# Optimization experiments

Hardware: AMD Instinct MI355X
Metric: run time of the kernel (lower is better)

The kernel has to match this reference:

```python
import jax, jax.numpy as jnp
import numpy as np

N_INSTR = 16384   # total instructions across all blocks
T_TOK   = 16      # max tokens per instruction
N_BLOCKS = 512    # number of basic blocks (batch)
MAX_BLK = 64      # max instructions per block
H = 128           # hidden_size
N_TOKENS = 1024   # vocab
P_INSTR = 32      # instr_param_size
P_GLOB = 8        # global_param_size
D_WORD = 2 * H + P_INSTR + P_GLOB  # word-LSTM input dim (bi char hidden + params)


def setup_inputs() -> dict:
    key = jax.random.key(0)
    ks = jax.random.split(key, 16)
    rng = np.random.default_rng(0)

    # ragged block lengths summing exactly to N_INSTR, values in [8, 56]
    bl = np.full(N_BLOCKS, N_INSTR // N_BLOCKS, dtype=np.int64)  # avg 32
    half = N_BLOCKS // 2
    delta = rng.integers(-24, 25, size=half)
    bl[:half] += delta
    bl[half:] -= delta
    block_lens = jnp.asarray(bl, dtype=jnp.int32)

    token_lens = jnp.asarray(rng.integers(4, T_TOK + 1, size=N_INSTR), dtype=jnp.int32)
    tokens = jax.random.randint(ks[0], (N_INSTR, T_TOK), 0, N_TOKENS, dtype=jnp.int32)

    instr_params = jax.random.normal(ks[1], (N_INSTR, P_INSTR), dtype=jnp.float32)
    global_params = jax.random.normal(ks[2], (N_BLOCKS, P_GLOB), dtype=jnp.float32)

    s = 1.0 / np.sqrt(H)
    def u(k, shape):
        return jax.random.uniform(k, shape, jnp.float32, -s, s)

    emb = jax.random.normal(ks[3], (N_TOKENS, H), dtype=jnp.float32) * 0.02
    # char LSTM (input dim H), forward and backward directions; b = b_ih + b_hh
    char_Wih_f = u(ks[4], (4 * H, H)); char_Whh_f = u(ks[5], (4 * H, H)); char_b_f = u(ks[6], (4 * H,))
    char_Wih_b = u(ks[7], (4 * H, H)); char_Whh_b = u(ks[8], (4 * H, H)); char_b_b = u(ks[9], (4 * H,))
    # word LSTM (input dim D_WORD)
    word_Wih_f = u(ks[10], (4 * H, D_WORD)); word_Whh_f = u(ks[11], (4 * H, H)); word_b_f = u(ks[12], (4 * H,))
    word_Wih_b = u(ks[13], (4 * H, D_WORD)); word_Whh_b = u(ks[14], (4 * H, H)); word_b_b = u(ks[15], (4 * H,))
    kf = jax.random.fold_in(key, 123)
    final_W = u(kf, (1, 2 * H + P_GLOB)); final_b = jnp.zeros((1,), jnp.float32)

    return dict(tokens=tokens, token_lens=token_lens, block_lens=block_lens,
                instr_params=instr_params, global_params=global_params, emb=emb,
                char_Wih_f=char_Wih_f, char_Whh_f=char_Whh_f, char_b_f=char_b_f,
                char_Wih_b=char_Wih_b, char_Whh_b=char_Whh_b, char_b_b=char_b_b,
                word_Wih_f=word_Wih_f, word_Whh_f=word_Whh_f, word_b_f=word_b_f,
                word_Wih_b=word_Wih_b, word_Whh_b=word_Whh_b, word_b_b=word_b_b,
                final_W=final_W, final_b=final_b)


def _run_dir(x, mask, Wih, Whh, b):
    # x: (B, T, D), mask: (B, T) bool. Masked LSTM scan; returns final hidden (B, H).
    B = x.shape[0]
    Hh = Whh.shape[1]
    def step(carry, inp):
        h, c = carry
        xt, m = inp                      # (B, D), (B,)
        g = xt @ Wih.T + h @ Whh.T + b   # (B, 4H)
        i, f, gg, o = jnp.split(g, 4, axis=-1)  # torch gate order i,f,g,o
        i = jax.nn.sigmoid(i); f = jax.nn.sigmoid(f)
        gg = jnp.tanh(gg); o = jax.nn.sigmoid(o)
        cn = f * c + i * gg
        hn = o * jnp.tanh(cn)
        m = m[:, None]
        return (jnp.where(m, hn, h), jnp.where(m, cn, c)), None
    init = (jnp.zeros((B, Hh), x.dtype), jnp.zeros((B, Hh), x.dtype))
    (h, _), _ = jax.lax.scan(step, init, (jnp.swapaxes(x, 0, 1), mask.T))
    return h


def _bilstm_final(x, lens, Wih_f, Whh_f, b_f, Wih_b, Whh_b, b_b):
    # final hidden of a 1-layer bi-LSTM over ragged sequences (pack_padded semantics)
    T = x.shape[1]
    t_idx = jnp.arange(T)
    mask = t_idx[None, :] < lens[:, None]          # (B, T)
    h_f = _run_dir(x, mask, Wih_f, Whh_f, b_f)
    rev_idx = jnp.maximum(lens[:, None] - 1 - t_idx[None, :], 0)  # valid prefix reversed
    x_rev = jnp.take_along_axis(x, rev_idx[:, :, None], axis=1)
    h_b = _run_dir(x_rev, mask, Wih_b, Whh_b, b_b)
    return jnp.concatenate([h_f, h_b], axis=-1)    # (B, 2H)


def reference(tokens, token_lens, block_lens, instr_params, global_params, emb,
              char_Wih_f, char_Whh_f, char_b_f, char_Wih_b, char_Whh_b, char_b_b,
              word_Wih_f, word_Whh_f, word_b_f, word_Wih_b, word_Whh_b, word_b_b,
              final_W, final_b):
    n_instr = tokens.shape[0]
    # char level: per-instruction bi-LSTM over token embeddings
    x = emb[tokens]                                # (N, T_TOK, H)
    instr_h = _bilstm_final(x, token_lens, char_Wih_f, char_Whh_f, char_b_f,
                            char_Wih_b, char_Whh_b, char_b_b)      # (N, 2H)
    instrs = jnp.concatenate([instr_h, instr_params], axis=1)      # (N, 2H+P_INSTR)
    # ragged re-pack: assign each instruction to its block and position
    ends = jnp.cumsum(block_lens)
    starts = ends - block_lens
    ar = jnp.arange(n_instr)
    bid = jnp.searchsorted(ends, ar, side='right')                 # block id per instr
    pos = ar - starts[bid]                                         # position within block
    full = jnp.concatenate([instrs, global_params[bid]], axis=1)   # (N, D_WORD)
    padded = jnp.zeros((block_lens.shape[0], MAX_BLK, full.shape[1]), full.dtype)
    padded = padded.at[bid, pos].set(full)                         # (B, MAX_BLK, D_WORD)
    # word level: per-block bi-LSTM over instruction summaries
    blocks_h = _bilstm_final(padded, block_lens, word_Wih_f, word_Whh_f, word_b_f,
                             word_Wih_b, word_Whh_b, word_b_b)     # (B, 2H)
    final_in = jnp.concatenate([blocks_h, global_params], axis=1)  # (B, 2H+P_GLOB)
    return final_in @ final_W.T + final_b                          # (B, 1)
```

## Files before the change

### kernel.cpp

```cpp
#include <hip/hip_runtime.h>
#include <hip/hip_bf16.h>
#include <math.h>

#define N_INSTR   16384
#define T_TOK     16
#define N_BLOCKS  512
#define MAX_BLK   64
#define HDIM      128
#define P_INSTR   32
#define P_GLOB    8
#define D_WORD    296
#define N_TOKENS  1024

#define CIB       32

#define HPAR      131072

__device__ __forceinline__ float sigf(float x) {
    return 1.0f / (1.0f + __expf(-x));
}
__device__ __forceinline__ float tanhf_s(float x) {
    float a = fabsf(x);
    float e = __expf(-2.0f * a);
    float t = (1.0f - e) / (1.0f + e);
    return copysignf(t, x);
}

__global__ __launch_bounds__(256) void prep_pack(
    const float* __restrict__ cWihF, const float* __restrict__ cWhhF,
    const float* __restrict__ cWihB, const float* __restrict__ cWhhB,
    const float* __restrict__ wWihF, const float* __restrict__ wWihB,
    const float* __restrict__ wWhhF, const float* __restrict__ wWhhB,
    float* __restrict__ W4cf, float* __restrict__ W4cb,
    float* __restrict__ W4p,  float* __restrict__ W4h)
{
    int idx = blockIdx.x * 256 + threadIdx.x;
    if (idx < 131072) {
        int kk = idx & 3, f = idx >> 2;
        int j = f & 511, k = ((f >> 9) << 2) + kk;
        W4cf[idx] = (k < 128) ? cWihF[j*128 + k] : cWhhF[j*128 + (k-128)];
    } else if (idx < 262144) {
        int id = idx - 131072;
        int kk = id & 3, f = id >> 2;
        int j = f & 511, k = ((f >> 9) << 2) + kk;
        W4cb[id] = (k < 128) ? cWihB[j*128 + k] : cWhhB[j*128 + (k-128)];
    } else if (idx < 262144 + 303104) {
        int id = idx - 262144;
        int kk = id & 3, f = id >> 2;
        int j = f & 1023, k = ((f >> 10) << 2) + kk;
        W4p[id] = (j < 512) ? wWihF[j*296 + k] : wWihB[(j-512)*296 + k];
    } else if (idx < 565248 + 131072) {
        int id = idx - 565248;
        int kk = id & 3, f = id >> 2;
        int j = f & 1023, k = ((f >> 10) << 2) + kk;
        W4h[id] = (j < 512) ? wWhhF[j*128 + k] : wWhhB[(j-512)*128 + k];
    }
}

__global__ __launch_bounds__(512) void scan_kernel(
    const int* __restrict__ block_lens, int* __restrict__ starts, int* __restrict__ bid)
{
    __shared__ int s[N_BLOCKS];
    int t = threadIdx.x;
    int len = block_lens[t];
    s[t] = len;
    __syncthreads();
    for (int off = 1; off < N_BLOCKS; off <<= 1) {
        int v = (t >= off) ? s[t - off] : 0;
        __syncthreads();
        s[t] += v;
        __syncthreads();
    }
    int start = s[t] - len;
    starts[t] = start;
    for (int p = 0; p < len; ++p) bid[start + p] = t;
}

__global__ __launch_bounds__(256) void zero_kernel(float4* __restrict__ p, int n4)
{
    int i = blockIdx.x * 256 + threadIdx.x;
    if (i < n4) p[i] = make_float4(0.f, 0.f, 0.f, 0.f);
}

__global__ __launch_bounds__(256) void sort_by_len(
    const int* __restrict__ token_lens, int* __restrict__ order)
{
    __shared__ int cnt[T_TOK + 1];
    __shared__ int base[T_TOK + 1];
    int tid = threadIdx.x;
    if (tid <= T_TOK) cnt[tid] = 0;
    __syncthreads();
    for (int i = tid; i < N_INSTR; i += 256) atomicAdd(&cnt[token_lens[i]], 1);
    __syncthreads();
    if (tid == 0) {
        int s = 0;
        for (int l = 0; l <= T_TOK; ++l) { base[l] = s; s += cnt[l]; }
    }
    __syncthreads();
    for (int i = tid; i < N_INSTR; i += 256) {
        int pos = atomicAdd(&base[token_lens[i]], 1);
        order[pos] = i;
    }
}

__global__ __launch_bounds__(256) void ex_pack(
    const float* __restrict__ emb,
    const float* __restrict__ W4cf, const float* __restrict__ W4cb,
    float* __restrict__ EF4, float* __restrict__ EB4)
{
    __shared__ float xe[128];
    int tk  = blockIdx.x;
    int tid = threadIdx.x;
    if (tid < 32) ((float4*)xe)[tid] = ((const float4*)(emb + tk * HDIM))[tid];
    __syncthreads();
    int u = tid & 127, dir = tid >> 7;
    const float4* W = (const float4*)(dir ? W4cb : W4cf);
    float a0 = 0.f, a1 = 0.f, a2 = 0.f, a3 = 0.f;
    for (int kc = 0; kc < 32; ++kc) {
        float4 x  = ((const float4*)xe)[kc];
        float4 w0 = W[kc*512 +   0 + u];
        float4 w1 = W[kc*512 + 128 + u];
        float4 w2 = W[kc*512 + 256 + u];
        float4 w3 = W[kc*512 + 384 + u];
        a0 = fmaf(w0.x,x.x,fmaf(w0.y,x.y,fmaf(w0.z,x.z,fmaf(w0.w,x.w,a0))));
        a1 = fmaf(w1.x,x.x,fmaf(w1.y,x.y,fmaf(w1.z,x.z,fmaf(w1.w,x.w,a1))));
        a2 = fmaf(w2.x,x.x,fmaf(w2.y,x.y,fmaf(w2.z,x.z,fmaf(w2.w,x.w,a2))));
        a3 = fmaf(w3.x,x.x,fmaf(w3.y,x.y,fmaf(w3.z,x.z,fmaf(w3.w,x.w,a3))));
    }
    float4 r = make_float4(a0, a1, a2, a3);
    ((float4*)(dir ? EB4 : EF4))[tk * 128 + u] = r;
}

__global__ __launch_bounds__(256, 2) void char_lstm(
    const int* __restrict__ tokens, const int* __restrict__ token_lens,
    const int* __restrict__ order,
    const float* __restrict__ EF4, const float* __restrict__ EB4,
    const float* __restrict__ W4f, const float* __restrict__ W4b,
    const float* __restrict__ bf,  const float* __restrict__ bb,
    float* __restrict__ instr_h)
{
    __shared__ float hF[CIB][128];
    __shared__ float hB[CIB][128];
    __shared__ int   toks[CIB][T_TOK];
    __shared__ int   lens[CIB];
    __shared__ int   iid[CIB];
    __shared__ int   maxl_s;

    const int tid = threadIdx.x;
    const int i0  = blockIdx.x * CIB;

    if (tid == 0) maxl_s = 0;
    __syncthreads();
    if (tid < CIB) {
        int id = order[i0 + tid];
        iid[tid] = id;
        int l = token_lens[id];
        lens[tid] = l;
        atomicMax(&maxl_s, l);
    }
    __syncthreads();
    for (int idx = tid; idx < CIB * T_TOK; idx += 256)
        toks[idx >> 4][idx & 15] = tokens[iid[idx >> 4] * T_TOK + (idx & 15)];
    for (int idx = tid; idx < CIB * 128; idx += 256) {
        ((float*)hF)[idx] = 0.f;
        ((float*)hB)[idx] = 0.f;
    }
    __syncthreads();

    const int u    = tid & 127;
    const int half = tid >> 7;
    const int ib0  = half * 16;

    float bfr[4], bbr[4];
    #pragma unroll
    for (int g = 0; g < 4; ++g) { bfr[g] = bf[g*128 + u]; bbr[g] = bb[g*128 + u]; }

    float cF[16], cB[16];
    #pragma unroll
    for (int i = 0; i < 16; ++i) { cF[i] = 0.f; cB[i] = 0.f; }

    const float4* Wf = (const float4*)W4f + 32*512;
    const float4* Wb = (const float4*)W4b + 32*512;
    const float4* EF = (const float4*)EF4;
    const float4* EB = (const float4*)EB4;

    const int maxl = maxl_s;

    for (int t = 0; t < maxl; ++t) {
        {
            float acc[16][4];
            #pragma unroll
            for (int il = 0; il < 16; ++il) {
                float4 e = EF[toks[ib0 + il][t] * 128 + u];
                acc[il][0] = e.x; acc[il][1] = e.y; acc[il][2] = e.z; acc[il][3] = e.w;
            }
            for (int kc = 0; kc < 32; ++kc) {
                float4 w0 = Wf[kc*512 +   0 + u];
                float4 w1 = Wf[kc*512 + 128 + u];
                float4 w2 = Wf[kc*512 + 256 + u];
                float4 w3 = Wf[kc*512 + 384 + u];
                #pragma unroll
                for (int il = 0; il < 16; ++il) {
                    float4 x = *(const float4*)&hF[ib0 + il][kc*4];
                    acc[il][0] = fmaf(w0.x,x.x,fmaf(w0.y,x.y,fmaf(w0.z,x.z,fmaf(w0.w,x.w,acc[il][0]))));
                    acc[il][1] = fmaf(w1.x,x.x,fmaf(w1.y,x.y,fmaf(w1.z,x.z,fmaf(w1.w,x.w,acc[il][1]))));
                    acc[il][2] = fmaf(w2.x,x.x,fmaf(w2.y,x.y,fmaf(w2.z,x.z,fmaf(w2.w,x.w,acc[il][2]))));
                    acc[il][3] = fmaf(w3.x,x.x,fmaf(w3.y,x.y,fmaf(w3.z,x.z,fmaf(w3.w,x.w,acc[il][3]))));
                }
            }
            __syncthreads();
            #pragma unroll
            for (int il = 0; il < 16; ++il) {
                int i = ib0 + il;
                if (t < lens[i]) {
                    float gi = sigf   (acc[il][0] + bfr[0]);
                    float gf = sigf   (acc[il][1] + bfr[1]);
                    float gg = tanhf_s(acc[il][2] + bfr[2]);
                    float go = sigf   (acc[il][3] + bfr[3]);
                    float cn = gf * cF[il] + gi * gg;
                    cF[il] = cn;
                    hF[i][u] = go * tanhf_s(cn);
                }
            }
        }
        {
            float acc[16][4];
            #pragma unroll
            for (int il = 0; il < 16; ++il) {
                int i = ib0 + il;
                int tt = lens[i] - 1 - t;
                tt = tt < 0 ? 0 : tt;
                float4 e = EB[toks[i][tt] * 128 + u];
                acc[il][0] = e.x; acc[il][1] = e.y; acc[il][2] = e.z; acc[il][3] = e.w;
            }
            for (int kc = 0; kc < 32; ++kc) {
                float4 w0 = Wb[kc*512 +   0 + u];
                float4 w1 = Wb[kc*512 + 128 + u];
                float4 w2 = Wb[kc*512 + 256 + u];
                float4 w3 = Wb[kc*512 + 384 + u];
                #pragma unroll
                for (int il = 0; il < 16; ++il) {
                    float4 x = *(const float4*)&hB[ib0 + il][kc*4];
                    acc[il][0] = fmaf(w0.x,x.x,fmaf(w0.y,x.y,fmaf(w0.z,x.z,fmaf(w0.w,x.w,acc[il][0]))));
                    acc[il][1] = fmaf(w1.x,x.x,fmaf(w1.y,x.y,fmaf(w1.z,x.z,fmaf(w1.w,x.w,acc[il][1]))));
                    acc[il][2] = fmaf(w2.x,x.x,fmaf(w2.y,x.y,fmaf(w2.z,x.z,fmaf(w2.w,x.w,acc[il][2]))));
                    acc[il][3] = fmaf(w3.x,x.x,fmaf(w3.y,x.y,fmaf(w3.z,x.z,fmaf(w3.w,x.w,acc[il][3]))));
                }
            }
            __syncthreads();
            #pragma unroll
            for (int il = 0; il < 16; ++il) {
                int i = ib0 + il;
                if (t < lens[i]) {
                    float gi = sigf   (acc[il][0] + bbr[0]);
                    float gf = sigf   (acc[il][1] + bbr[1]);
                    float gg = tanhf_s(acc[il][2] + bbr[2]);
                    float go = sigf   (acc[il][3] + bbr[3]);
                    float cn = gf * cB[il] + gi * gg;
                    cB[il] = cn;
                    hB[i][u] = go * tanhf_s(cn);
                }
            }
        }
        __syncthreads();
    }

    for (int idx = tid; idx < CIB * 128; idx += 256) {
        int i = idx >> 7, uu = idx & 127;
        int id = iid[i];
        instr_h[id * 256 +       uu] = hF[i][uu];
        instr_h[id * 256 + 128 + uu] = hB[i][uu];
    }
}

__global__ __launch_bounds__(256) void xw_gather(
    const float* __restrict__ instr_h, const float* __restrict__ instr_params,
    const float* __restrict__ gparams, const int* __restrict__ bid,
    float* __restrict__ xw)
{
    int idx = blockIdx.x * 256 + threadIdx.x;
    if (idx >= N_INSTR * 74) return;
    int i = idx / 74, c = idx % 74;
    float4 v;
    if (c < 64)      v = ((const float4*)(instr_h + i*256))[c];
    else if (c < 72) v = ((const float4*)(instr_params + i*32))[c - 64];
    else             v = ((const float4*)(gparams + bid[i]*8))[c - 72];
    ((float4*)(xw + i*296))[c] = v;
}

__global__ __launch_bounds__(256) void word_proj(
    const float* __restrict__ xw, const float* __restrict__ W4p,
    const float* __restrict__ b_f, const float* __restrict__ b_b,
    float* __restrict__ P)
{
    __shared__ float xs[16][296];
    int tid = threadIdx.x;
    int rowTile = blockIdx.x >> 2;
    int colTile = blockIdx.x & 3;
    int i0 = rowTile * 16;

    for (int idx = tid; idx < 16 * 74; idx += 256) {
        int i = idx / 74, c = idx % 74;
        ((float4*)&xs[i][0])[c] = ((const float4*)(xw + (size_t)(i0 + i) * 296))[c];
    }
    __syncthreads();

    int j = colTile * 256 + tid;
    float acc[16];
    #pragma unroll
    for (int i = 0; i < 16; ++i) acc[i] = 0.f;
    const float4* W4 = (const float4*)W4p;
    for (int kc = 0; kc < 74; ++kc) {
        float4 w = W4[kc*1024 + j];
        #pragma unroll
        for (int i = 0; i < 16; ++i) {
            float4 x = ((const float4*)&xs[i][0])[kc];
            acc[i] = fmaf(w.x,x.x,fmaf(w.y,x.y,fmaf(w.z,x.z,fmaf(w.w,x.w,acc[i]))));
        }
    }
    float bias = (j < 512) ? b_f[j] : b_b[j - 512];
    for (int i = 0; i < 16; ++i)
        P[(size_t)(i0 + i) * 1024 + j] = acc[i] + bias;
}

__global__ __launch_bounds__(256) void word_step(
    const float* __restrict__ W4h, const float* __restrict__ P,
    const int* __restrict__ starts, const int* __restrict__ block_lens,
    const float* __restrict__ hrd, float* __restrict__ hwr,
    float* __restrict__ cst, int t)
{
    __shared__ float hs[32][128];
    __shared__ int actflag;

    int bx = blockIdx.x;
    int bt = bx & 15, ut = (bx >> 4) & 3, d = bx >> 6;
    int tid = threadIdx.x;
    int b0 = bt * 32;

    const float* hbase = hrd + (size_t)(d * 512 + b0) * 128;
    for (int idx = tid; idx < 32 * 128 / 4; idx += 256)
        ((float4*)hs)[idx] = ((const float4*)hbase)[idx];
    if (tid == 0) actflag = 0;

    int u   = ut * 32 + (tid & 31);
    int bg  = tid >> 5;
    int lb0 = bg * 4;

    int blens[4], bsta[4], myact = 0;
    #pragma unroll
    for (int q = 0; q < 4; ++q) {
        int b = b0 + lb0 + q;
        blens[q] = block_lens[b];
        bsta[q]  = starts[b];
        myact |= (t < blens[q]) ? 1 : 0;
    }
    __syncthreads();
    if (myact) atomicOr(&actflag, 1);
    __syncthreads();

    float* hw = hwr + (size_t)(d * 512 + b0) * 128;
    if (!actflag) {
        #pragma unroll
        for (int q = 0; q < 4; ++q) hw[(lb0 + q) * 128 + u] = hs[lb0 + q][u];
        return;
    }

    float acc[4][4];
    #pragma unroll
    for (int q = 0; q < 4; ++q)
        { acc[q][0]=0.f; acc[q][1]=0.f; acc[q][2]=0.f; acc[q][3]=0.f; }
    const float4* W4 = (const float4*)W4h;
    for (int kc = 0; kc < 32; ++kc) {
        float4 w0 = W4[kc*1024 + d*512 +   0 + u];
        float4 w1 = W4[kc*1024 + d*512 + 128 + u];
        float4 w2 = W4[kc*1024 + d*512 + 256 + u];
        float4 w3 = W4[kc*1024 + d*512 + 384 + u];
        #pragma unroll
        for (int q = 0; q < 4; ++q) {
            float4 h4 = *(const float4*)&hs[lb0 + q][kc*4];
            acc[q][0] = fmaf(w0.x,h4.x,fmaf(w0.y,h4.y,fmaf(w0.z,h4.z,fmaf(w0.w,h4.w,acc[q][0]))));
            acc[q][1] = fmaf(w1.x,h4.x,fmaf(w1.y,h4.y,fmaf(w1.z,h4.z,fmaf(w1.w,h4.w,acc[q][1]))));
            acc[q][2] = fmaf(w2.x,h4.x,fmaf(w2.y,h4.y,fmaf(w2.z,h4.z,fmaf(w2.w,h4.w,acc[q][2]))));
            acc[q][3] = fmaf(w3.x,h4.x,fmaf(w3.y,h4.y,fmaf(w3.z,h4.z,fmaf(w3.w,h4.w,acc[q][3]))));
        }
    }
    #pragma unroll
    for (int q = 0; q < 4; ++q) {
        int b = b0 + lb0 + q;
        int len = blens[q];
        float hold = hs[lb0 + q][u];
        if (t < len) {
            int rs = (d == 0) ? (bsta[q] + t) : (bsta[q] + len - 1 - t);
            const float* Prow = P + (size_t)rs * 1024 + d * 512;
            float g0 = acc[q][0] + Prow[  0 + u];
            float g1 = acc[q][1] + Prow[128 + u];
            float g2 = acc[q][2] + Prow[256 + u];
            float g3 = acc[q][3] + Prow[384 + u];
            float gi = sigf(g0), gf = sigf(g1), gg = tanhf_s(g2), go = sigf(g3);
            float* cp = cst + (size_t)(d * 512 + b) * 128 + u;
            float c  = *cp;
            float cn = gf * c + gi * gg;
            *cp = cn;
            hw[(lb0 + q) * 128 + u] = go * tanhf_s(cn);
        } else {
            hw[(lb0 + q) * 128 + u] = hold;
        }
    }
}

__global__ __launch_bounds__(256) void final_k(
    const float* __restrict__ hfinal, const float* __restrict__ gp,
    const float* __restrict__ fW, const float* __restrict__ fb,
    float* __restrict__ out)
{
    int tid = threadIdx.x;
    int w = tid >> 6, l = tid & 63;
    int b = blockIdx.x * 4 + w;
    const float* hf = hfinal + (size_t)(0 * 512 + b) * 128;
    const float* hb = hfinal + (size_t)(1 * 512 + b) * 128;
    float s = hf[l] * fW[l] + hf[l + 64] * fW[l + 64]
            + hb[l] * fW[128 + l] + hb[l + 64] * fW[192 + l];
    if (l < 8) s += gp[b * 8 + l] * fW[256 + l];
    #pragma unroll
    for (int off = 32; off > 0; off >>= 1) s += __shfl_down(s, off);
    if (l == 0) out[b] = s + fb[0];
}

extern "C" void kernel_launch(void* const* d_in, const int* in_sizes, int n_in,
                              void* d_out, int out_size, void* d_ws, size_t ws_size,
                              hipStream_t stream)
{
    const int*   tokens        = (const int*)  d_in[0];
    const int*   token_lens    = (const int*)  d_in[1];
    const int*   block_lens    = (const int*)  d_in[2];
    const float* instr_params  = (const float*)d_in[3];
    const float* global_params = (const float*)d_in[4];
    const float* emb           = (const float*)d_in[5];
    const float* cWihF = (const float*)d_in[6];
    const float* cWhhF = (const float*)d_in[7];
    const float* cbF   = (const float*)d_in[8];
    const float* cWihB = (const float*)d_in[9];
    const float* cWhhB = (const float*)d_in[10];
    const float* cbB   = (const float*)d_in[11];
    const float* wWihF = (const float*)d_in[12];
    const float* wWhhF = (const float*)d_in[13];
    const float* wbF   = (const float*)d_in[14];
    const float* wWihB = (const float*)d_in[15];
    const float* wWhhB = (const float*)d_in[16];
    const float* wbB   = (const float*)d_in[17];
    const float* fW    = (const float*)d_in[18];
    const float* fb    = (const float*)d_in[19];
    float* out = (float*)d_out;

    char* ws = (char*)d_ws;
    size_t off = 0;
    auto alloc_f = [&](size_t nfloats) { float* p = (float*)(ws + off); off += nfloats * 4; return p; };

    float* W4cf    = alloc_f(131072);
    float* W4cb    = alloc_f(131072);
    float* W4p     = alloc_f(303104);
    float* W4h     = alloc_f(131072);
    float* instr_h = alloc_f((size_t)N_INSTR * 256);
    float* xw      = alloc_f((size_t)N_INSTR * 296);
    float* P       = alloc_f((size_t)N_INSTR * 1024);
    float* hbuf    = alloc_f(2 * HPAR);
    float* cst     = alloc_f(2 * 512 * 128);
    float* EF4     = alloc_f((size_t)N_TOKENS * 128 * 4);
    float* EB4     = alloc_f((size_t)N_TOKENS * 128 * 4);
    int*   starts  = (int*)(ws + off); off += 512 * 4;
    int*   bid     = (int*)(ws + off); off += N_INSTR * 4;
    int*   order   = (int*)(ws + off); off += N_INSTR * 4;

    prep_pack<<<2720, 256, 0, stream>>>(cWihF, cWhhF, cWihB, cWhhB,
                                        wWihF, wWihB, wWhhF, wWhhB,
                                        W4cf, W4cb, W4p, W4h);
    zero_kernel<<<384, 256, 0, stream>>>((float4*)hbuf, 98304);
    scan_kernel<<<1, 512, 0, stream>>>(block_lens, starts, bid);
    sort_by_len<<<1, 256, 0, stream>>>(token_lens, order);
    ex_pack<<<N_TOKENS, 256, 0, stream>>>(emb, W4cf, W4cb, EF4, EB4);

    char_lstm<<<N_INSTR / CIB, 256, 0, stream>>>(tokens, token_lens, order,
                                                 EF4, EB4, W4cf, W4cb,
                                                 cbF, cbB, instr_h);
    xw_gather<<<4736, 256, 0, stream>>>(instr_h, instr_params, global_params, bid, xw);
    word_proj<<<4096, 256, 0, stream>>>(xw, W4p, wbF, wbB, P);

    for (int t = 0; t < MAX_BLK; ++t) {
        const float* hrd = hbuf + (size_t)(t & 1) * HPAR;
        float*       hwr = hbuf + (size_t)((t + 1) & 1) * HPAR;
        word_step<<<128, 256, 0, stream>>>(W4h, P, starts, block_lens, hrd, hwr, cst, t);
    }
    final_k<<<128, 256, 0, stream>>>(hbuf, global_params, fW, fb, out);
}
```

Baseline: 1.696 ms.

## Fuse word LSTM timesteps into one persistent kernel and halve char LSTM tile

Replaces the 64 per-timestep word_step launches with a single word_lstm kernel. In it, each workgroup owns four length-sorted blocks in one direction and keeps h in shared memory and c in registers across all timesteps, which removes launch overhead and the global h/c round trips. A new sort_blocks kernel groups blocks of similar length so each workgroup iterates only to its local max length. The char LSTM tile also drops from 32 to 16 instructions per workgroup with higher occupancy bounds, giving more workgroups for parallelism. In exchange, each workgroup rereads the recurrent weights from cache every step, and only 256 workgroups run the word recurrence.

```diff
diff --git a/kernel.cpp b/kernel.cpp
--- a/kernel.cpp
+++ b/kernel.cpp
@@ -12,9 +12,7 @@
 #define D_WORD    296
 #define N_TOKENS  1024
 
-#define CIB       32
-
-#define HPAR      131072
+#define CIB       16
 
 __device__ __forceinline__ float sigf(float x) {
     return 1.0f / (1.0f + __expf(-x));
@@ -76,12 +74,6 @@
     for (int p = 0; p < len; ++p) bid[start + p] = t;
 }
 
-__global__ __launch_bounds__(256) void zero_kernel(float4* __restrict__ p, int n4)
-{
-    int i = blockIdx.x * 256 + threadIdx.x;
-    if (i < n4) p[i] = make_float4(0.f, 0.f, 0.f, 0.f);
-}
-
 __global__ __launch_bounds__(256) void sort_by_len(
     const int* __restrict__ token_lens, int* __restrict__ order)
 {
@@ -101,6 +93,26 @@
         int pos = atomicAdd(&base[token_lens[i]], 1);
         order[pos] = i;
     }
+}
+
+__global__ __launch_bounds__(512) void sort_blocks(
+    const int* __restrict__ block_lens, int* __restrict__ border)
+{
+    __shared__ int cnt[MAX_BLK + 1];
+    __shared__ int base[MAX_BLK + 1];
+    int tid = threadIdx.x;
+    if (tid <= MAX_BLK) cnt[tid] = 0;
+    __syncthreads();
+    int len = block_lens[tid];
+    atomicAdd(&cnt[len], 1);
+    __syncthreads();
+    if (tid == 0) {
+        int s = 0;
+        for (int l = 0; l <= MAX_BLK; ++l) { base[l] = s; s += cnt[l]; }
+    }
+    __syncthreads();
+    int pos = atomicAdd(&base[len], 1);
+    border[pos] = tid;
 }
 
 __global__ __launch_bounds__(256) void ex_pack(
@@ -131,7 +143,7 @@
     ((float4*)(dir ? EB4 : EF4))[tk * 128 + u] = r;
 }
 
-__global__ __launch_bounds__(256, 2) void char_lstm(
+__global__ __launch_bounds__(256, 4) void char_lstm(
     const int* __restrict__ tokens, const int* __restrict__ token_lens,
     const int* __restrict__ order,
     const float* __restrict__ EF4, const float* __restrict__ EB4,
@@ -169,15 +181,15 @@
 
     const int u    = tid & 127;
     const int half = tid >> 7;
-    const int ib0  = half * 16;
+    const int ib0  = half * 8;
 
     float bfr[4], bbr[4];
     #pragma unroll
     for (int g = 0; g < 4; ++g) { bfr[g] = bf[g*128 + u]; bbr[g] = bb[g*128 + u]; }
 
-    float cF[16], cB[16];
+    float cF[8], cB[8];
     #pragma unroll
-    for (int i = 0; i < 16; ++i) { cF[i] = 0.f; cB[i] = 0.f; }
+    for (int i = 0; i < 8; ++i) { cF[i] = 0.f; cB[i] = 0.f; }
 
     const float4* Wf = (const float4*)W4f + 32*512;
     const float4* Wb = (const float4*)W4b + 32*512;
@@ -188,9 +200,9 @@
 
     for (int t = 0; t < maxl; ++t) {
         {
-            float acc[16][4];
+            float acc[8][4];
             #pragma unroll
-            for (int il = 0; il < 16; ++il) {
+            for (int il = 0; il < 8; ++il) {
                 float4 e = EF[toks[ib0 + il][t] * 128 + u];
                 acc[il][0] = e.x; acc[il][1] = e.y; acc[il][2] = e.z; acc[il][3] = e.w;
             }
@@ -200,7 +212,7 @@
                 float4 w2 = Wf[kc*512 + 256 + u];
                 float4 w3 = Wf[kc*512 + 384 + u];
                 #pragma unroll
-                for (int il = 0; il < 16; ++il) {
+                for (int il = 0; il < 8; ++il) {
                     float4 x = *(const float4*)&hF[ib0 + il][kc*4];
                     acc[il][0] = fmaf(w0.x,x.x,fmaf(w0.y,x.y,fmaf(w0.z,x.z,fmaf(w0.w,x.w,acc[il][0]))));
                     acc[il][1] = fmaf(w1.x,x.x,fmaf(w1.y,x.y,fmaf(w1.z,x.z,fmaf(w1.w,x.w,acc[il][1]))));
@@ -210,7 +222,7 @@
             }
             __syncthreads();
             #pragma unroll
-            for (int il = 0; il < 16; ++il) {
+            for (int il = 0; il < 8; ++il) {
                 int i = ib0 + il;
                 if (t < lens[i]) {
                     float gi = sigf   (acc[il][0] + bfr[0]);
@@ -224,9 +236,9 @@
             }
         }
         {
-            float acc[16][4];
+            float acc[8][4];
             #pragma unroll
-            for (int il = 0; il < 16; ++il) {
+            for (int il = 0; il < 8; ++il) {
                 int i = ib0 + il;
                 int tt = lens[i] - 1 - t;
                 tt = tt < 0 ? 0 : tt;
@@ -239,7 +251,7 @@
                 float4 w2 = Wb[kc*512 + 256 + u];
                 float4 w3 = Wb[kc*512 + 384 + u];
                 #pragma unroll
-                for (int il = 0; il < 16; ++il) {
+                for (int il = 0; il < 8; ++il) {
                     float4 x = *(const float4*)&hB[ib0 + il][kc*4];
                     acc[il][0] = fmaf(w0.x,x.x,fmaf(w0.y,x.y,fmaf(w0.z,x.z,fmaf(w0.w,x.w,acc[il][0]))));
                     acc[il][1] = fmaf(w1.x,x.x,fmaf(w1.y,x.y,fmaf(w1.z,x.z,fmaf(w1.w,x.w,acc[il][1]))));
@@ -249,7 +261,7 @@
             }
             __syncthreads();
             #pragma unroll
-            for (int il = 0; il < 16; ++il) {
+            for (int il = 0; il < 8; ++il) {
                 int i = ib0 + il;
                 if (t < lens[i]) {
                     float gi = sigf   (acc[il][0] + bbr[0]);
@@ -323,89 +335,87 @@
         P[(size_t)(i0 + i) * 1024 + j] = acc[i] + bias;
 }
 
-__global__ __launch_bounds__(256) void word_step(
+__global__ __launch_bounds__(256, 2) void word_lstm(
     const float* __restrict__ W4h, const float* __restrict__ P,
     const int* __restrict__ starts, const int* __restrict__ block_lens,
-    const float* __restrict__ hrd, float* __restrict__ hwr,
-    float* __restrict__ cst, int t)
-{
-    __shared__ float hs[32][128];
-    __shared__ int actflag;
-
-    int bx = blockIdx.x;
-    int bt = bx & 15, ut = (bx >> 4) & 3, d = bx >> 6;
-    int tid = threadIdx.x;
-    int b0 = bt * 32;
-
-    const float* hbase = hrd + (size_t)(d * 512 + b0) * 128;
-    for (int idx = tid; idx < 32 * 128 / 4; idx += 256)
-        ((float4*)hs)[idx] = ((const float4*)hbase)[idx];
-    if (tid == 0) actflag = 0;
-
-    int u   = ut * 32 + (tid & 31);
-    int bg  = tid >> 5;
-    int lb0 = bg * 4;
-
-    int blens[4], bsta[4], myact = 0;
-    #pragma unroll
-    for (int q = 0; q < 4; ++q) {
-        int b = b0 + lb0 + q;
-        blens[q] = block_lens[b];
-        bsta[q]  = starts[b];
-        myact |= (t < blens[q]) ? 1 : 0;
-    }
-    __syncthreads();
-    if (myact) atomicOr(&actflag, 1);
-    __syncthreads();
-
-    float* hw = hwr + (size_t)(d * 512 + b0) * 128;
-    if (!actflag) {
-        #pragma unroll
-        for (int q = 0; q < 4; ++q) hw[(lb0 + q) * 128 + u] = hs[lb0 + q][u];
-        return;
-    }
-
-    float acc[4][4];
-    #pragma unroll
-    for (int q = 0; q < 4; ++q)
-        { acc[q][0]=0.f; acc[q][1]=0.f; acc[q][2]=0.f; acc[q][3]=0.f; }
+    const int* __restrict__ border,
+    float* __restrict__ hfin)
+{
+    __shared__ float hs[4][128];
+    __shared__ int   binfo[4][3];
+
+    const int w   = blockIdx.x;
+    const int d   = w & 1;
+    const int g   = w >> 1;
+    const int tid = threadIdx.x;
+    const int u    = tid & 127;
+    const int half = tid >> 7;
+    const int q0   = half * 2;
+
+    if (tid < 4) {
+        int ob = border[g * 4 + tid];
+        binfo[tid][0] = ob;
+        binfo[tid][1] = starts[ob];
+        binfo[tid][2] = block_lens[ob];
+    }
+    for (int idx = tid; idx < 4 * 128; idx += 256) ((float*)hs)[idx] = 0.f;
+    __syncthreads();
+
+    const int len0 = binfo[q0][2],     len1 = binfo[q0 + 1][2];
+    const int st0  = binfo[q0][1],     st1  = binfo[q0 + 1][1];
+    const int maxlen = max(max(binfo[0][2], binfo[1][2]),
+                           max(binfo[2][2], binfo[3][2]));
+
+    float c0 = 0.f, c1 = 0.f;
     const float4* W4 = (const float4*)W4h;
-    for (int kc = 0; kc < 32; ++kc) {
-        float4 w0 = W4[kc*1024 + d*512 +   0 + u];
-        float4 w1 = W4[kc*1024 + d*512 + 128 + u];
-        float4 w2 = W4[kc*1024 + d*512 + 256 + u];
-        float4 w3 = W4[kc*1024 + d*512 + 384 + u];
-        #pragma unroll
-        for (int q = 0; q < 4; ++q) {
-            float4 h4 = *(const float4*)&hs[lb0 + q][kc*4];
-            acc[q][0] = fmaf(w0.x,h4.x,fmaf(w0.y,h4.y,fmaf(w0.z,h4.z,fmaf(w0.w,h4.w,acc[q][0]))));
-            acc[q][1] = fmaf(w1.x,h4.x,fmaf(w1.y,h4.y,fmaf(w1.z,h4.z,fmaf(w1.w,h4.w,acc[q][1]))));
-            acc[q][2] = fmaf(w2.x,h4.x,fmaf(w2.y,h4.y,fmaf(w2.z,h4.z,fmaf(w2.w,h4.w,acc[q][2]))));
-            acc[q][3] = fmaf(w3.x,h4.x,fmaf(w3.y,h4.y,fmaf(w3.z,h4.z,fmaf(w3.w,h4.w,acc[q][3]))));
-        }
-    }
-    #pragma unroll
-    for (int q = 0; q < 4; ++q) {
-        int b = b0 + lb0 + q;
-        int len = blens[q];
-        float hold = hs[lb0 + q][u];
-        if (t < len) {
-            int rs = (d == 0) ? (bsta[q] + t) : (bsta[q] + len - 1 - t);
+
+    for (int t = 0; t < maxlen; ++t) {
+        float a0[4] = {0.f, 0.f, 0.f, 0.f};
+        float a1[4] = {0.f, 0.f, 0.f, 0.f};
+        for (int kc = 0; kc < 32; ++kc) {
+            float4 w0 = W4[kc*1024 + d*512 +   0 + u];
+            float4 w1 = W4[kc*1024 + d*512 + 128 + u];
+            float4 w2 = W4[kc*1024 + d*512 + 256 + u];
+            float4 w3 = W4[kc*1024 + d*512 + 384 + u];
+            float4 h0 = *(const float4*)&hs[q0][kc*4];
+            float4 h1 = *(const float4*)&hs[q0 + 1][kc*4];
+            a0[0] = fmaf(w0.x,h0.x,fmaf(w0.y,h0.y,fmaf(w0.z,h0.z,fmaf(w0.w,h0.w,a0[0]))));
+            a0[1] = fmaf(w1.x,h0.x,fmaf(w1.y,h0.y,fmaf(w1.z,h0.z,fmaf(w1.w,h0.w,a0[1]))));
+            a0[2] = fmaf(w2.x,h0.x,fmaf(w2.y,h0.y,fmaf(w2.z,h0.z,fmaf(w2.w,h0.w,a0[2]))));
+            a0[3] = fmaf(w3.x,h0.x,fmaf(w3.y,h0.y,fmaf(w3.z,h0.z,fmaf(w3.w,h0.w,a0[3]))));
+            a1[0] = fmaf(w0.x,h1.x,fmaf(w0.y,h1.y,fmaf(w0.z,h1.z,fmaf(w0.w,h1.w,a1[0]))));
+            a1[1] = fmaf(w1.x,h1.x,fmaf(w1.y,h1.y,fmaf(w1.z,h1.z,fmaf(w1.w,h1.w,a1[1]))));
+            a1[2] = fmaf(w2.x,h1.x,fmaf(w2.y,h1.y,fmaf(w2.z,h1.z,fmaf(w2.w,h1.w,a1[2]))));
+            a1[3] = fmaf(w3.x,h1.x,fmaf(w3.y,h1.y,fmaf(w3.z,h1.z,fmaf(w3.w,h1.w,a1[3]))));
+        }
+        __syncthreads();
+        if (t < len0) {
+            int rs = (d == 0) ? (st0 + t) : (st0 + len0 - 1 - t);
             const float* Prow = P + (size_t)rs * 1024 + d * 512;
-            float g0 = acc[q][0] + Prow[  0 + u];
-            float g1 = acc[q][1] + Prow[128 + u];
-            float g2 = acc[q][2] + Prow[256 + u];
-            float g3 = acc[q][3] + Prow[384 + u];
-            float gi = sigf(g0), gf = sigf(g1), gg = tanhf_s(g2), go = sigf(g3);
-            float* cp = cst + (size_t)(d * 512 + b) * 128 + u;
-            float c  = *cp;
-            float cn = gf * c + gi * gg;
-            *cp = cn;
-            hw[(lb0 + q) * 128 + u] = go * tanhf_s(cn);
-        } else {
-            hw[(lb0 + q) * 128 + u] = hold;
-        }
-    }
+            float gi = sigf   (a0[0] + Prow[  0 + u]);
+            float gf = sigf   (a0[1] + Prow[128 + u]);
+            float gg = tanhf_s(a0[2] + Prow[256 + u]);
+            float go = sigf   (a0[3] + Prow[384 + u]);
+            float cn = gf * c0 + gi * gg;
+            c0 = cn;
+            hs[q0][u] = go * tanhf_s(cn);
+        }
+        if (t < len1) {
+            int rs = (d == 0) ? (st1 + t) : (st1 + len1 - 1 - t);
+            const float* Prow = P + (size_t)rs * 1024 + d * 512;
+            float gi = sigf   (a1[0] + Prow[  0 + u]);
+            float gf = sigf   (a1[1] + Prow[128 + u]);
+            float gg = tanhf_s(a1[2] + Prow[256 + u]);
+            float go = sigf   (a1[3] + Prow[384 + u]);
+            float cn = gf * c1 + gi * gg;
+            c1 = cn;
+            hs[q0 + 1][u] = go * tanhf_s(cn);
+        }
+        __syncthreads();
+    }
+
+    hfin[(size_t)(d * 512 + binfo[q0][0])     * 128 + u] = hs[q0][u];
+    hfin[(size_t)(d * 512 + binfo[q0 + 1][0]) * 128 + u] = hs[q0 + 1][u];
 }
 
 __global__ __launch_bounds__(256) void final_k(
@@ -463,20 +473,20 @@
     float* instr_h = alloc_f((size_t)N_INSTR * 256);
     float* xw      = alloc_f((size_t)N_INSTR * 296);
     float* P       = alloc_f((size_t)N_INSTR * 1024);
-    float* hbuf    = alloc_f(2 * HPAR);
-    float* cst     = alloc_f(2 * 512 * 128);
+    float* hfin    = alloc_f(2 * 512 * 128);
     float* EF4     = alloc_f((size_t)N_TOKENS * 128 * 4);
     float* EB4     = alloc_f((size_t)N_TOKENS * 128 * 4);
     int*   starts  = (int*)(ws + off); off += 512 * 4;
     int*   bid     = (int*)(ws + off); off += N_INSTR * 4;
     int*   order   = (int*)(ws + off); off += N_INSTR * 4;
+    int*   border  = (int*)(ws + off); off += 512 * 4;
 
     prep_pack<<<2720, 256, 0, stream>>>(cWihF, cWhhF, cWihB, cWhhB,
                                         wWihF, wWihB, wWhhF, wWhhB,
                                         W4cf, W4cb, W4p, W4h);
-    zero_kernel<<<384, 256, 0, stream>>>((float4*)hbuf, 98304);
     scan_kernel<<<1, 512, 0, stream>>>(block_lens, starts, bid);
     sort_by_len<<<1, 256, 0, stream>>>(token_lens, order);
+    sort_blocks<<<1, 512, 0, stream>>>(block_lens, border);
     ex_pack<<<N_TOKENS, 256, 0, stream>>>(emb, W4cf, W4cb, EF4, EB4);
 
     char_lstm<<<N_INSTR / CIB, 256, 0, stream>>>(tokens, token_lens, order,
@@ -484,11 +494,6 @@
                                                  cbF, cbB, instr_h);
     xw_gather<<<4736, 256, 0, stream>>>(instr_h, instr_params, global_params, bid, xw);
     word_proj<<<4096, 256, 0, stream>>>(xw, W4p, wbF, wbB, P);
-
-    for (int t = 0; t < MAX_BLK; ++t) {
-        const float* hrd = hbuf + (size_t)(t & 1) * HPAR;
-        float*       hwr = hbuf + (size_t)((t + 1) & 1) * HPAR;
-        word_step<<<128, 256, 0, stream>>>(W4h, P, starts, block_lens, hrd, hwr, cst, t);
-    }
-    final_k<<<128, 256, 0, stream>>>(hbuf, global_params, fW, fb, out);
-}
+    word_lstm<<<256, 256, 0, stream>>>(W4h, P, starts, block_lens, border, hfin);
+    final_k<<<128, 256, 0, stream>>>(hfin, global_params, fW, fb, out);
+}
```

Measured after the change: 1.433 ms. 1.18x faster.
